# Kernel optimization log

Measured on AMD Instinct MI355X. Metric: run time of the kernel, lower is better.

## Reference

```python
import jax, jax.numpy as jnp
import numpy as np

N = 2_000_000   # total nodes
B = 8192        # graphs (segments)
NEURONS = 64
GLOBAL_D = 103
HID = 32


def setup_inputs() -> dict:
    key = jax.random.key(0)
    ks = jax.random.split(key, 8)
    x = jax.random.normal(ks[0], (N, NEURONS), dtype=jnp.float32)
    # sorted graph ids, as produced by PyG batching; with N >> B all graphs are present
    node_batch = jnp.sort(jax.random.randint(ks[1], (N,), 0, B, dtype=jnp.int64))
    global_fea = jax.random.normal(ks[2], (B, GLOBAL_D), dtype=jnp.float32)
    # node_layer1: Linear(neurons+103 -> 32); atten_layer: Linear(32 -> 1)
    D = NEURONS + GLOBAL_D
    W1 = jax.random.normal(ks[3], (D, HID), dtype=jnp.float32) / np.sqrt(D)
    b1 = jnp.zeros((HID,), dtype=jnp.float32)
    W2 = jax.random.normal(ks[4], (HID, 1), dtype=jnp.float32) / np.sqrt(HID)
    b2 = jnp.zeros((1,), dtype=jnp.float32)
    return {"x": x, "node_batch": node_batch, "global_fea": global_fea,
            "W1": W1, "b1": b1, "W2": W2, "b2": b2}


def reference(x, node_batch, global_fea, W1, b1, W2, b2):
    # repeat_interleave(global_fea, counts) with sorted node_batch covering all
    # graph ids == a plain gather by node_batch
    graph_embed = global_fea[node_batch]                      # [N, 103]
    chunk = jnp.concatenate([x, graph_embed], axis=-1)        # [N, 167]
    h = jax.nn.softplus(chunk @ W1 + b1)                      # [N, 32]
    logits = h @ W2 + b2                                      # [N, 1]
    # segment-wise (per-graph) numerically stable softmax over nodes
    seg = node_batch
    lmax = jax.ops.segment_max(logits, seg, num_segments=B)   # [B, 1]
    e = jnp.exp(logits - lmax[seg])                           # [N, 1]
    ssum = jax.ops.segment_sum(e, seg, num_segments=B)        # [B, 1]
    weights = e / ssum[seg]                                   # [N, 1]
    return weights
```

## Files before the change

kernel.cpp:

```cpp
#include <hip/hip_runtime.h>
#include <math.h>

#define NEURONS 64
#define HID 32
#define GD 103
#define TW 16
#define NCHUNK (NEURONS / TW)
#define PAD 17
#define ROWS 256

__global__ __launch_bounds__(256) void k_gpart(
    const float* __restrict__ gf, const float* __restrict__ W1,
    const float* __restrict__ b1, float* __restrict__ gpart, int B)
{
    int t = blockIdx.x * 256 + threadIdx.x;
    if (t >= B * HID) return;
    int b = t >> 5;
    int h = t & 31;
    float acc = b1[h];
    const float* grow = gf + (size_t)b * GD;
    for (int d = 0; d < GD; ++d)
        acc = fmaf(grow[d], W1[(NEURONS + d) * HID + h], acc);
    gpart[t] = acc;
}

__global__ __launch_bounds__(256) void k_bounds(
    const int* __restrict__ nb, int* __restrict__ start, int n, int B)
{
    int b = blockIdx.x * 256 + threadIdx.x;
    if (b > B) return;
    if (b == B) { start[B] = n; return; }
    int lo = 0, hi = n;
    while (lo < hi) {
        int mid = (lo + hi) >> 1;
        if (nb[mid] < b) lo = mid + 1; else hi = mid;
    }
    start[b] = lo;
}

__global__ __launch_bounds__(256) void k_logits(
    const float* __restrict__ x, const int* __restrict__ nb,
    const float* __restrict__ gpart, const float* __restrict__ W1,
    const float* __restrict__ W2, const float* __restrict__ b2,
    float* __restrict__ logits, int n)
{
    __shared__ float xs[2][ROWS * PAD];

    const int tid = threadIdx.x;
    const long base = (long)blockIdx.x * ROWS;
    const long i = base + tid;
    const bool alive = i < (long)n;

    int seg = alive ? nb[i] : 0;

    float acc[HID];
    const float4* gp = (const float4*)(gpart + (size_t)seg * HID);
    #pragma unroll
    for (int q = 0; q < HID / 4; ++q) {
        float4 v = gp[q];
        acc[4 * q + 0] = v.x; acc[4 * q + 1] = v.y;
        acc[4 * q + 2] = v.z; acc[4 * q + 3] = v.w;
    }

    float4 pre[4];
    #pragma unroll
    for (int k = 0; k < 4; ++k) {
        int p = tid + 256 * k;
        long r = base + (p >> 2);
        if (r >= n) r = n - 1;
        pre[k] = *(const float4*)(x + r * NEURONS + (p & 3) * 4);
    }

    for (int c = 0; c < NCHUNK; ++c) {
        float* buf = xs[c & 1];
        #pragma unroll
        for (int k = 0; k < 4; ++k) {
            int p = tid + 256 * k;
            float* dst = buf + (p >> 2) * PAD + (p & 3) * 4;
            dst[0] = pre[k].x; dst[1] = pre[k].y;
            dst[2] = pre[k].z; dst[3] = pre[k].w;
        }
        __syncthreads();

        if (c < NCHUNK - 1) {
            #pragma unroll
            for (int k = 0; k < 4; ++k) {
                int p = tid + 256 * k;
                long r = base + (p >> 2);
                if (r >= n) r = n - 1;
                pre[k] = *(const float4*)(x + r * NEURONS + (c + 1) * TW + (p & 3) * 4);
            }
        }

        const float* xrow = xs[c & 1] + tid * PAD;
        const float* w = W1 + c * TW * HID;
        #pragma unroll
        for (int d = 0; d < TW; ++d) {
            float xd = xrow[d];
            #pragma unroll
            for (int h = 0; h < HID; ++h)
                acc[h] = fmaf(xd, w[d * HID + h], acc[h]);
        }
        __syncthreads();
    }

    if (!alive) return;

    float logit = b2[0];
    #pragma unroll
    for (int h = 0; h < HID; ++h) {
        float z = acc[h];
        float sp = fmaxf(z, 0.0f) + __logf(1.0f + __expf(-fabsf(z)));
        logit = fmaf(sp, W2[h], logit);
    }
    logits[i] = logit;
}

__device__ __forceinline__ float wave_max(float v) {
    #pragma unroll
    for (int o = 32; o > 0; o >>= 1) v = fmaxf(v, __shfl_down(v, o, 64));
    return v;
}
__device__ __forceinline__ float wave_sum(float v) {
    #pragma unroll
    for (int o = 32; o > 0; o >>= 1) v += __shfl_down(v, o, 64);
    return v;
}

__global__ __launch_bounds__(256) void k_seg(
    const float* __restrict__ logits, const int* __restrict__ start,
    float* __restrict__ out)
{
    int b = blockIdx.x;
    int s = start[b], e = start[b + 1];
    int tid = threadIdx.x;
    int wid = tid >> 6;

    __shared__ float sm[4];

    float m = -INFINITY;
    for (int i = s + tid; i < e; i += 256) m = fmaxf(m, logits[i]);
    m = wave_max(m);
    if ((tid & 63) == 0) sm[wid] = m;
    __syncthreads();
    float bm = fmaxf(fmaxf(sm[0], sm[1]), fmaxf(sm[2], sm[3]));
    __syncthreads();

    float sum = 0.0f;
    for (int i = s + tid; i < e; i += 256) sum += __expf(logits[i] - bm);
    sum = wave_sum(sum);
    if ((tid & 63) == 0) sm[wid] = sum;
    __syncthreads();
    float inv = 1.0f / (sm[0] + sm[1] + sm[2] + sm[3]);

    for (int i = s + tid; i < e; i += 256)
        out[i] = __expf(logits[i] - bm) * inv;
}

extern "C" void kernel_launch(void* const* d_in, const int* in_sizes, int n_in,
                              void* d_out, int out_size, void* d_ws, size_t ws_size,
                              hipStream_t stream)
{
    const float* x   = (const float*)d_in[0];
    const int*   nb  = (const int*)d_in[1];
    const float* gf  = (const float*)d_in[2];
    const float* W1  = (const float*)d_in[3];
    const float* b1  = (const float*)d_in[4];
    const float* W2  = (const float*)d_in[5];
    const float* b2  = (const float*)d_in[6];
    float* out = (float*)d_out;

    const int N = in_sizes[1];
    const int B = in_sizes[2] / GD;

    float* gpart  = (float*)d_ws;
    float* logits = gpart + (size_t)B * HID;
    int*   start  = (int*)(logits + N);

    int gp_blocks = (B * HID + 255) / 256;
    k_gpart<<<gp_blocks, 256, 0, stream>>>(gf, W1, b1, gpart, B);

    int bd_blocks = (B + 1 + 255) / 256;
    k_bounds<<<bd_blocks, 256, 0, stream>>>(nb, start, N, B);

    int n_blocks = (N + ROWS - 1) / ROWS;
    k_logits<<<n_blocks, 256, 0, stream>>>(x, nb, gpart, W1, W2, b2, logits, N);

    k_seg<<<B, 256, 0, stream>>>(logits, start, out);
}
```

Measured before the change: 730.2 us.

## Fuse per-node logits into per-segment softmax kernel, merge prep kernels

Folds the gpart and bounds kernels into one launch with a block-index split. Replaces the separate logits and segment-softmax kernels with one per-graph kernel that computes logits for its own nodes, keeps them in shared memory when the segment fits, and runs the softmax in place. This removes the round trip of logits through global memory and two launches. In exchange, each thread now reads x rows directly (strided float4 loads, no shared-memory staging), segments of about 244 nodes leave most of each 256-thread block idle, and W1 reads come from global or cache rather than a coalesced tile.

```diff
diff --git a/kernel.cpp b/kernel.cpp
--- a/kernel.cpp
+++ b/kernel.cpp
@@ -4,116 +4,36 @@
 #define NEURONS 64
 #define HID 32
 #define GD 103
-#define TW 16
-#define NCHUNK (NEURONS / TW)
-#define PAD 17
-#define ROWS 256
+#define CAP 1024
 
-__global__ __launch_bounds__(256) void k_gpart(
+__global__ __launch_bounds__(256) void k_prep(
     const float* __restrict__ gf, const float* __restrict__ W1,
-    const float* __restrict__ b1, float* __restrict__ gpart, int B)
+    const float* __restrict__ b1, const int* __restrict__ nb,
+    float* __restrict__ gpart, int* __restrict__ start,
+    int n, int B, int gp_blocks)
 {
-    int t = blockIdx.x * 256 + threadIdx.x;
-    if (t >= B * HID) return;
-    int b = t >> 5;
-    int h = t & 31;
-    float acc = b1[h];
-    const float* grow = gf + (size_t)b * GD;
-    for (int d = 0; d < GD; ++d)
-        acc = fmaf(grow[d], W1[(NEURONS + d) * HID + h], acc);
-    gpart[t] = acc;
-}
-
-__global__ __launch_bounds__(256) void k_bounds(
-    const int* __restrict__ nb, int* __restrict__ start, int n, int B)
-{
-    int b = blockIdx.x * 256 + threadIdx.x;
-    if (b > B) return;
-    if (b == B) { start[B] = n; return; }
-    int lo = 0, hi = n;
-    while (lo < hi) {
-        int mid = (lo + hi) >> 1;
-        if (nb[mid] < b) lo = mid + 1; else hi = mid;
+    if ((int)blockIdx.x < gp_blocks) {
+        int t = blockIdx.x * 256 + threadIdx.x;
+        if (t >= B * HID) return;
+        int b = t >> 5;
+        int h = t & 31;
+        float acc = b1[h];
+        const float* grow = gf + (size_t)b * GD;
+        #pragma unroll
+        for (int d = 0; d < GD; ++d)
+            acc = fmaf(grow[d], W1[(NEURONS + d) * HID + h], acc);
+        gpart[t] = acc;
+    } else {
+        int b = (blockIdx.x - gp_blocks) * 256 + threadIdx.x;
+        if (b > B) return;
+        if (b == B) { start[B] = n; return; }
+        int lo = 0, hi = n;
+        while (lo < hi) {
+            int mid = (lo + hi) >> 1;
+            if (nb[mid] < b) lo = mid + 1; else hi = mid;
+        }
+        start[b] = lo;
     }
-    start[b] = lo;
-}
-
-__global__ __launch_bounds__(256) void k_logits(
-    const float* __restrict__ x, const int* __restrict__ nb,
-    const float* __restrict__ gpart, const float* __restrict__ W1,
-    const float* __restrict__ W2, const float* __restrict__ b2,
-    float* __restrict__ logits, int n)
-{
-    __shared__ float xs[2][ROWS * PAD];
-
-    const int tid = threadIdx.x;
-    const long base = (long)blockIdx.x * ROWS;
-    const long i = base + tid;
-    const bool alive = i < (long)n;
-
-    int seg = alive ? nb[i] : 0;
-
-    float acc[HID];
-    const float4* gp = (const float4*)(gpart + (size_t)seg * HID);
-    #pragma unroll
-    for (int q = 0; q < HID / 4; ++q) {
-        float4 v = gp[q];
-        acc[4 * q + 0] = v.x; acc[4 * q + 1] = v.y;
-        acc[4 * q + 2] = v.z; acc[4 * q + 3] = v.w;
-    }
-
-    float4 pre[4];
-    #pragma unroll
-    for (int k = 0; k < 4; ++k) {
-        int p = tid + 256 * k;
-        long r = base + (p >> 2);
-        if (r >= n) r = n - 1;
-        pre[k] = *(const float4*)(x + r * NEURONS + (p & 3) * 4);
-    }
-
-    for (int c = 0; c < NCHUNK; ++c) {
-        float* buf = xs[c & 1];
-        #pragma unroll
-        for (int k = 0; k < 4; ++k) {
-            int p = tid + 256 * k;
-            float* dst = buf + (p >> 2) * PAD + (p & 3) * 4;
-            dst[0] = pre[k].x; dst[1] = pre[k].y;
-            dst[2] = pre[k].z; dst[3] = pre[k].w;
-        }
-        __syncthreads();
-
-        if (c < NCHUNK - 1) {
-            #pragma unroll
-            for (int k = 0; k < 4; ++k) {
-                int p = tid + 256 * k;
-                long r = base + (p >> 2);
-                if (r >= n) r = n - 1;
-                pre[k] = *(const float4*)(x + r * NEURONS + (c + 1) * TW + (p & 3) * 4);
-            }
-        }
-
-        const float* xrow = xs[c & 1] + tid * PAD;
-        const float* w = W1 + c * TW * HID;
-        #pragma unroll
-        for (int d = 0; d < TW; ++d) {
-            float xd = xrow[d];
-            #pragma unroll
-            for (int h = 0; h < HID; ++h)
-                acc[h] = fmaf(xd, w[d * HID + h], acc[h]);
-        }
-        __syncthreads();
-    }
-
-    if (!alive) return;
-
-    float logit = b2[0];
-    #pragma unroll
-    for (int h = 0; h < HID; ++h) {
-        float z = acc[h];
-        float sp = fmaxf(z, 0.0f) + __logf(1.0f + __expf(-fabsf(z)));
-        logit = fmaf(sp, W2[h], logit);
-    }
-    logits[i] = logit;
 }
 
 __device__ __forceinline__ float wave_max(float v) {
@@ -127,64 +47,126 @@
     return v;
 }
 
-__global__ __launch_bounds__(256) void k_seg(
-    const float* __restrict__ logits, const int* __restrict__ start,
-    float* __restrict__ out)
+__global__ __launch_bounds__(256) void k_fused(
+    const float* __restrict__ x, const float* __restrict__ gpart,
+    const float* __restrict__ W1, const float* __restrict__ W2,
+    const float* __restrict__ b2, const int* __restrict__ start,
+    float* __restrict__ out, float* __restrict__ lg_ws)
 {
-    int b = blockIdx.x;
-    int s = start[b], e = start[b + 1];
-    int tid = threadIdx.x;
-    int wid = tid >> 6;
+    __shared__ float slog[CAP];
+    __shared__ float sred[4];
 
-    __shared__ float sm[4];
+    const int b = blockIdx.x;
+    const int s = start[b];
+    const int e = start[b + 1];
+    const int len = e - s;
+    if (len <= 0) return;
+    const int tid = threadIdx.x;
+    const int wid = tid >> 6;
 
-    float m = -INFINITY;
-    for (int i = s + tid; i < e; i += 256) m = fmaxf(m, logits[i]);
-    m = wave_max(m);
-    if ((tid & 63) == 0) sm[wid] = m;
-    __syncthreads();
-    float bm = fmaxf(fmaxf(sm[0], sm[1]), fmaxf(sm[2], sm[3]));
+    float binit[HID], w2r[HID];
+    const float* gp = gpart + (size_t)b * HID;
+    #pragma unroll
+    for (int h = 0; h < HID; ++h) binit[h] = gp[h];
+    #pragma unroll
+    for (int h = 0; h < HID; ++h) w2r[h] = W2[h];
+    const float b2v = b2[0];
+
+    const bool fits = (len <= CAP);
+
+    for (int i = s + tid; i < e; i += 256) {
+        const float4* __restrict__ xr = (const float4*)(x + (size_t)i * NEURONS);
+        float acc[HID];
+        #pragma unroll
+        for (int h = 0; h < HID; ++h) acc[h] = binit[h];
+        #pragma unroll
+        for (int q = 0; q < NEURONS / 4; ++q) {
+            const float4 v = xr[q];
+            const float* __restrict__ w = W1 + q * 4 * HID;
+            #pragma unroll
+            for (int h = 0; h < HID; ++h) acc[h] = fmaf(v.x, w[h],           acc[h]);
+            #pragma unroll
+            for (int h = 0; h < HID; ++h) acc[h] = fmaf(v.y, w[HID + h],     acc[h]);
+            #pragma unroll
+            for (int h = 0; h < HID; ++h) acc[h] = fmaf(v.z, w[2 * HID + h], acc[h]);
+            #pragma unroll
+            for (int h = 0; h < HID; ++h) acc[h] = fmaf(v.w, w[3 * HID + h], acc[h]);
+        }
+        float logit = b2v;
+        #pragma unroll
+        for (int h = 0; h < HID; ++h) {
+            float z = acc[h];
+            float sp = fmaxf(z, 0.0f) + __logf(1.0f + __expf(-fabsf(z)));
+            logit = fmaf(sp, w2r[h], logit);
+        }
+        if (fits) slog[i - s] = logit;
+        else      lg_ws[i] = logit;
+    }
     __syncthreads();
 
-    float sum = 0.0f;
-    for (int i = s + tid; i < e; i += 256) sum += __expf(logits[i] - bm);
-    sum = wave_sum(sum);
-    if ((tid & 63) == 0) sm[wid] = sum;
-    __syncthreads();
-    float inv = 1.0f / (sm[0] + sm[1] + sm[2] + sm[3]);
+    if (fits) {
+        float m = -INFINITY;
+        for (int j = tid; j < len; j += 256) m = fmaxf(m, slog[j]);
+        m = wave_max(m);
+        if ((tid & 63) == 0) sred[wid] = m;
+        __syncthreads();
+        const float bm = fmaxf(fmaxf(sred[0], sred[1]), fmaxf(sred[2], sred[3]));
+        __syncthreads();
 
-    for (int i = s + tid; i < e; i += 256)
-        out[i] = __expf(logits[i] - bm) * inv;
+        float sum = 0.0f;
+        for (int j = tid; j < len; j += 256) sum += __expf(slog[j] - bm);
+        sum = wave_sum(sum);
+        if ((tid & 63) == 0) sred[wid] = sum;
+        __syncthreads();
+        const float inv = 1.0f / (sred[0] + sred[1] + sred[2] + sred[3]);
+
+        for (int j = tid; j < len; j += 256)
+            out[s + j] = __expf(slog[j] - bm) * inv;
+    } else {
+        const float* lg = lg_ws + s;
+        float m = -INFINITY;
+        for (int j = tid; j < len; j += 256) m = fmaxf(m, lg[j]);
+        m = wave_max(m);
+        if ((tid & 63) == 0) sred[wid] = m;
+        __syncthreads();
+        const float bm = fmaxf(fmaxf(sred[0], sred[1]), fmaxf(sred[2], sred[3]));
+        __syncthreads();
+
+        float sum = 0.0f;
+        for (int j = tid; j < len; j += 256) sum += __expf(lg[j] - bm);
+        sum = wave_sum(sum);
+        if ((tid & 63) == 0) sred[wid] = sum;
+        __syncthreads();
+        const float inv = 1.0f / (sred[0] + sred[1] + sred[2] + sred[3]);
+
+        for (int j = tid; j < len; j += 256)
+            out[s + j] = __expf(lg[j] - bm) * inv;
+    }
 }
 
 extern "C" void kernel_launch(void* const* d_in, const int* in_sizes, int n_in,
                               void* d_out, int out_size, void* d_ws, size_t ws_size,
                               hipStream_t stream)
 {
-    const float* x   = (const float*)d_in[0];
-    const int*   nb  = (const int*)d_in[1];
-    const float* gf  = (const float*)d_in[2];
-    const float* W1  = (const float*)d_in[3];
-    const float* b1  = (const float*)d_in[4];
-    const float* W2  = (const float*)d_in[5];
-    const float* b2  = (const float*)d_in[6];
+    const float* x  = (const float*)d_in[0];
+    const int*   nb = (const int*)d_in[1];
+    const float* gf = (const float*)d_in[2];
+    const float* W1 = (const float*)d_in[3];
+    const float* b1 = (const float*)d_in[4];
+    const float* W2 = (const float*)d_in[5];
+    const float* b2 = (const float*)d_in[6];
     float* out = (float*)d_out;
 
     const int N = in_sizes[1];
     const int B = in_sizes[2] / GD;
 
-    float* gpart  = (float*)d_ws;
-    float* logits = gpart + (size_t)B * HID;
-    int*   start  = (int*)(logits + N);
+    float* gpart = (float*)d_ws;
+    int*   start = (int*)(gpart + (size_t)B * HID);
+    float* lg_ws = (float*)(start + (B + 2));
 
-    int gp_blocks = (B * HID + 255) / 256;
-    k_gpart<<<gp_blocks, 256, 0, stream>>>(gf, W1, b1, gpart, B);
-
-    int bd_blocks = (B + 1 + 255) / 256;
-    k_bounds<<<bd_blocks, 256, 0, stream>>>(nb, start, N, B);
-
-    int n_blocks = (N + ROWS - 1) / ROWS;
-    k_logits<<<n_blocks, 256, 0, stream>>>(x, nb, gpart, W1, W2, b2, logits, N);
-
-    k_seg<<<B, 256, 0, stream>>>(logits, start, out);
+    const int gp_blocks = (B * HID + 255) / 256;
+    const int bd_blocks = (B + 1 + 255) / 256;
+    k_prep<<<gp_blocks + bd_blocks, 256, 0, stream>>>(gf, W1, b1, nb, gpart, start,
+                                                      N, B, gp_blocks);
+    k_fused<<<B, 256, 0, stream>>>(x, gpart, W1, W2, b2, start, out, lg_ws);
 }
```

New measurement: 971.8 us. 33.1% more time.
